# Kernel optimization log

Hardware: AMD Instinct MI355X
Metric: run time of the kernel (lower is better)

Reference implementation:

```python
import jax, jax.numpy as jnp
import numpy as np

# static config (matches init_kwargs)
H, W = 56, 56
T = 4            # temporal_dims
C = 256          # dim1
NH = 8           # num_heads
WS = 7           # window_size
SS = 3           # shift_size
HID = 1024       # mlp hidden = 4*C
N = WS * WS      # tokens per window
EPS = 1e-5


def _ln(x, g, b):
    m = jnp.mean(x, axis=-1, keepdims=True)
    v = jnp.mean((x - m) ** 2, axis=-1, keepdims=True)
    return (x - m) * jax.lax.rsqrt(v + EPS) * g + b


def _window_partition(x, ws):
    B, Hh, Ww, Cc = x.shape
    x = x.reshape(B, Hh // ws, ws, Ww // ws, ws, Cc)
    return x.transpose(0, 1, 3, 2, 4, 5).reshape(-1, ws, ws, Cc)


def _window_reverse(win, ws, Hh, Ww):
    B = win.shape[0] // ((Hh // ws) * (Ww // ws))
    x = win.reshape(B, Hh // ws, Ww // ws, ws, ws, -1)
    return x.transpose(0, 1, 3, 2, 4, 5).reshape(B, Hh, Ww, -1)


def _rel_pos_index(ws):
    coords = np.stack(np.meshgrid(np.arange(ws), np.arange(ws), indexing='ij'))
    cf = coords.reshape(2, -1)
    rel = (cf[:, :, None] - cf[:, None, :]).transpose(1, 2, 0).astype(np.int64)
    rel[..., 0] += ws - 1
    rel[..., 1] += ws - 1
    rel[..., 0] *= 2 * ws - 1
    return rel.sum(-1)  # (ws*ws, ws*ws)


def _shift_mask():
    # identical to the torch buffer built in __init__ (on temporal_dims*H x W grid)
    img = np.zeros((T * H, W), dtype=np.float32)
    cnt = 0
    for hs in (slice(0, -WS), slice(-WS, -SS), slice(-SS, None)):
        for wsl in (slice(0, -WS), slice(-WS, -SS), slice(-SS, None)):
            img[hs, wsl] = cnt
            cnt += 1
    mw = img.reshape((T * H) // WS, WS, W // WS, WS).transpose(0, 2, 1, 3).reshape(-1, N)
    am = mw[:, None, :] - mw[:, :, None]
    return np.where(am != 0, np.float32(-100.0), np.float32(0.0))  # (nW, N, N)

_RPI = _rel_pos_index(WS)
_ATTN_MASK = _shift_mask()


def setup_inputs() -> dict:
    key = jax.random.key(0)
    ks = jax.random.split(key, 8)
    B = 4
    s = 0.02
    return {
        'x1': jax.random.normal(ks[0], (B, T * H * W, C), jnp.float32),
        'x2': jax.random.normal(ks[1], (B, H * W, C), jnp.float32),
        'norm1_g': jnp.ones((C,), jnp.float32),
        'norm1_b': jnp.zeros((C,), jnp.float32),
        'qkv_w': jax.random.normal(ks[2], (3 * C, C), jnp.float32) * s,
        'qkv_b': jnp.zeros((3 * C,), jnp.float32),
        'proj_w': jax.random.normal(ks[3], (C, C), jnp.float32) * s,
        'proj_b': jnp.zeros((C,), jnp.float32),
        'rpb_table': jax.random.normal(ks[4], ((2 * WS - 1) ** 2, NH), jnp.float32) * s,
        'norm2_g': jnp.ones((C,), jnp.float32),
        'norm2_b': jnp.zeros((C,), jnp.float32),
        'fc1_w': jax.random.normal(ks[5], (HID, C), jnp.float32) * s,
        'fc1_b': jnp.zeros((HID,), jnp.float32),
        'fc2_w': jax.random.normal(ks[6], (C, HID), jnp.float32) * s,
        'fc2_b': jnp.zeros((C,), jnp.float32),
    }


def _block(x1, norm1_g, norm1_b, qkv_w, qkv_b, proj_w, proj_b, rpb_table,
           norm2_g, norm2_b, fc1_w, fc1_b, fc2_w, fc2_b):
    B, L, _ = x1.shape
    hd = C // NH
    shortcut = x1
    x = _ln(x1, norm1_g, norm1_b).reshape(B, T * H, W, C)
    # cyclic shift + window partition
    x = jnp.roll(x, shift=(-SS, -SS), axis=(1, 2))
    xw = _window_partition(x, WS).reshape(-1, N, C)          # (B*nW, N, C)
    Bw = xw.shape[0]
    nW = Bw // B
    # window attention with relative position bias + shift mask
    qkv = (xw @ qkv_w.T + qkv_b).reshape(Bw, N, 3, NH, hd).transpose(2, 0, 3, 1, 4)
    q, k, v = qkv[0], qkv[1], qkv[2]
    attn = jnp.einsum('bhnd,bhmd->bhnm', q * (hd ** -0.5), k)
    bias = rpb_table[jnp.asarray(_RPI)].transpose(2, 0, 1)    # (NH, N, N)
    attn = attn + bias[None]
    mask = jnp.asarray(_ATTN_MASK)
    attn = attn.reshape(B, nW, NH, N, N) + mask[None, :, None]
    attn = jax.nn.softmax(attn.reshape(Bw, NH, N, N), axis=-1)
    y = jnp.einsum('bhnm,bhmd->bhnd', attn, v).transpose(0, 2, 1, 3).reshape(Bw, N, C)
    y = y @ proj_w.T + proj_b
    # reverse windows + un-shift
    y = _window_reverse(y.reshape(-1, WS, WS, C), WS, T * H, W)
    y = jnp.roll(y, shift=(SS, SS), axis=(1, 2)).reshape(B, L, C)
    out = y
    x1 = shortcut + y
    # MLP (GELU exact, as torch nn.GELU default)
    h = _ln(x1, norm2_g, norm2_b)
    h = jax.nn.gelu(h @ fc1_w.T + fc1_b, approximate=False)
    x1 = x1 + (h @ fc2_w.T + fc2_b)
    return x1, out


def reference(x1, x2, norm1_g, norm1_b, qkv_w, qkv_b, proj_w, proj_b, rpb_table,
              norm2_g, norm2_b, fc1_w, fc1_b, fc2_w, fc2_b):
    # last_view=True: x2 is reshaped but unused by the executed path
    return _block(x1, norm1_g, norm1_b, qkv_w, qkv_b, proj_w, proj_b, rpb_table,
                  norm2_g, norm2_b, fc1_w, fc1_b, fc2_w, fc2_b)
```

## Files before the change

kernel.cpp:

```cpp
#include <hip/hip_runtime.h>
#include <hip/hip_bf16.h>
#include <cmath>

#define CDIM 256
#define TPW 49
#define NWIN 1024
#define MTOK (NWIN * TPW)
#define NHEAD 8
#define GH 224
#define GW 56
#define PLD 72

typedef __attribute__((ext_vector_type(8))) __bf16 bf16x8;
typedef __attribute__((ext_vector_type(4))) float f32x4;

__device__ __forceinline__ __bf16 to_bf16(float f) {
    __hip_bfloat16 h = __float2bfloat16(f);
    return *(__bf16*)&h;
}

__device__ __forceinline__ void async_copy16(const void* g, void* l) {
    __builtin_amdgcn_global_load_lds(
        (const __attribute__((address_space(1))) void*)g,
        (__attribute__((address_space(3))) void*)l, 16, 0, 0);
}

__device__ __forceinline__ float wave_sum(float v) {
    v += __shfl_down(v, 32);
    v += __shfl_down(v, 16);
    v += __shfl_down(v, 8);
    v += __shfl_down(v, 4);
    v += __shfl_down(v, 2);
    v += __shfl_down(v, 1);
    return v;
}

__global__ __launch_bounds__(256) void castall_kernel(
    const float* __restrict__ qw, const float* __restrict__ pw,
    const float* __restrict__ f1, const float* __restrict__ f2,
    __hip_bfloat16* __restrict__ dst)
{
    const int i = blockIdx.x * 256 + threadIdx.x;
    float v;
    if (i < 196608) v = qw[i];
    else if (i < 262144) v = pw[i - 196608];
    else if (i < 524288) v = f1[i - 262144];
    else v = f2[i - 524288];
    dst[i] = __float2bfloat16(v);
}

__global__ __launch_bounds__(256) void cb_kernel(
    const float* __restrict__ rpb, float* __restrict__ cbt)
{
    const int cls = blockIdx.x >> 3, head = blockIdx.x & 7;
    for (int e = threadIdx.x; e < 64 * 64; e += 256) {
        const int m = e >> 6, n = e & 63;
        float v;
        if (m >= 49 || n >= 49) v = -30000.0f;
        else {
            const int in_ = n / 7, jn = n - in_ * 7;
            const int im = m / 7, jm = m - im * 7;
            v = rpb[((in_ - im + 6) * 13 + (jn - jm + 6)) * 8 + head];
            const int hn = (cls & 2) ? 217 + in_ : in_;
            const int wn = (cls & 1) ? 49 + jn : jn;
            const int hm = (cls & 2) ? 217 + im : im;
            const int wm = (cls & 1) ? 49 + jm : jm;
            const int rn = (hn < 217 ? 0 : (hn < 221 ? 3 : 6)) + (wn < 49 ? 0 : (wn < 53 ? 1 : 2));
            const int rm = (hm < 217 ? 0 : (hm < 221 ? 3 : 6)) + (wm < 49 ? 0 : (wm < 53 ? 1 : 2));
            if (rn != rm) v -= 100.0f;
        }
        cbt[((long)blockIdx.x * 64 + m) * 64 + n] = v;
    }
}

__global__ __launch_bounds__(256) void ln1_window_kernel(
    const float* __restrict__ x1, const float* __restrict__ g,
    const float* __restrict__ b, __hip_bfloat16* __restrict__ out)
{
    const int wave = threadIdx.x >> 6, lane = threadIdx.x & 63;
    const int t = blockIdx.x * 4 + wave;
    const int bw = t / TPW, n = t - bw * TPW;
    const int bb = bw >> 8, wi = bw & 255;
    const int hb = wi >> 3, wb = wi & 7;
    const int i = n / 7, j = n - i * 7;
    int h0 = hb * 7 + i + 3; if (h0 >= GH) h0 -= GH;
    int w0 = wb * 7 + j + 3; if (w0 >= GW) w0 -= GW;
    const long src = ((long)(bb * GH + h0) * GW + w0) * CDIM + lane * 4;
    const float4 v = *(const float4*)(x1 + src);
    float s = v.x + v.y + v.z + v.w;
    s = wave_sum(s);
    const float mean = __shfl(s, 0) * (1.0f / 256.0f);
    const float4 d = { v.x - mean, v.y - mean, v.z - mean, v.w - mean };
    float s2 = d.x * d.x + d.y * d.y + d.z * d.z + d.w * d.w;
    s2 = wave_sum(s2);
    const float rstd = rsqrtf(__shfl(s2, 0) * (1.0f / 256.0f) + 1e-5f);
    const float4 g4 = *(const float4*)(g + lane * 4);
    const float4 b4 = *(const float4*)(b + lane * 4);
    short4 pk;
    { __bf16 h = to_bf16(d.x * rstd * g4.x + b4.x); pk.x = *(short*)&h; }
    { __bf16 h = to_bf16(d.y * rstd * g4.y + b4.y); pk.y = *(short*)&h; }
    { __bf16 h = to_bf16(d.z * rstd * g4.z + b4.z); pk.z = *(short*)&h; }
    { __bf16 h = to_bf16(d.w * rstd * g4.w + b4.w); pk.w = *(short*)&h; }
    *(short4*)((short*)out + (long)t * CDIM + lane * 4) = pk;
}

__global__ __launch_bounds__(256) void ln_kernel(
    const float* __restrict__ x, const float* __restrict__ g,
    const float* __restrict__ b, __hip_bfloat16* __restrict__ out)
{
    const int wave = threadIdx.x >> 6, lane = threadIdx.x & 63;
    const long t = (long)blockIdx.x * 4 + wave;
    const float4 v = *(const float4*)(x + t * CDIM + lane * 4);
    float s = v.x + v.y + v.z + v.w;
    s = wave_sum(s);
    const float mean = __shfl(s, 0) * (1.0f / 256.0f);
    const float4 d = { v.x - mean, v.y - mean, v.z - mean, v.w - mean };
    float s2 = d.x * d.x + d.y * d.y + d.z * d.z + d.w * d.w;
    s2 = wave_sum(s2);
    const float rstd = rsqrtf(__shfl(s2, 0) * (1.0f / 256.0f) + 1e-5f);
    const float4 g4 = *(const float4*)(g + lane * 4);
    const float4 b4 = *(const float4*)(b + lane * 4);
    short4 pk;
    { __bf16 h = to_bf16(d.x * rstd * g4.x + b4.x); pk.x = *(short*)&h; }
    { __bf16 h = to_bf16(d.y * rstd * g4.y + b4.y); pk.y = *(short*)&h; }
    { __bf16 h = to_bf16(d.z * rstd * g4.z + b4.z); pk.z = *(short*)&h; }
    { __bf16 h = to_bf16(d.w * rstd * g4.w + b4.w); pk.w = *(short*)&h; }
    *(short4*)((short*)out + t * CDIM + lane * 4) = pk;
}

template <int EPI, typename OutT>
__global__ __launch_bounds__(256) void gemm_mfma(
    const __hip_bfloat16* __restrict__ X, const __hip_bfloat16* __restrict__ W,
    const float* __restrict__ bias, OutT* __restrict__ Y,
    int M, int K, int N, const float* __restrict__ res, float* __restrict__ Y2)
{
    __shared__ __hip_bfloat16 As[128 * 32];
    __shared__ __hip_bfloat16 Bs[128 * 32];
    const int tid = threadIdx.x;
    const int wave = tid >> 6, lane = tid & 63;
    const int nwg = gridDim.x * gridDim.y;
    const int L = blockIdx.y * gridDim.x + blockIdx.x;
    const int cpx = nwg >> 3;
    const int orig = (L & 7) * cpx + (L >> 3);
    const int bxx = orig % gridDim.x;
    const int byy = orig / gridDim.x;
    const int bm = byy * 128, bn = bxx * 128;
    const int wm = (wave & 1) * 64, wn = (wave >> 1) * 64;
    const int m16 = lane & 15, quad = lane >> 4;
    const int srow = lane >> 2;
    const int scol = (lane & 3) * 8;

    f32x4 acc[4][4] = {};

    for (int k0 = 0; k0 < K; k0 += 32) {
#pragma unroll
        for (int j = 0; j < 2; ++j) {
            const int rg = wave * 2 + j;
            const int row = rg * 16 + srow;
            async_copy16(X + (long)(bm + row) * K + k0 + scol, (char*)As + rg * 1024);
            async_copy16(W + (long)(bn + row) * K + k0 + scol, (char*)Bs + rg * 1024);
        }
        __syncthreads();
        bf16x8 af[4], bf[4];
#pragma unroll
        for (int i = 0; i < 4; ++i)
            af[i] = *(const bf16x8*)&As[(wm + i * 16 + m16) * 32 + quad * 8];
#pragma unroll
        for (int j = 0; j < 4; ++j)
            bf[j] = *(const bf16x8*)&Bs[(wn + j * 16 + m16) * 32 + quad * 8];
#pragma unroll
        for (int i = 0; i < 4; ++i)
#pragma unroll
            for (int j = 0; j < 4; ++j)
                acc[i][j] = __builtin_amdgcn_mfma_f32_16x16x32_bf16(bf[j], af[i], acc[i][j], 0, 0, 0);
        __syncthreads();
    }

#pragma unroll
    for (int i = 0; i < 4; ++i) {
        const long row = bm + wm + i * 16 + m16;
        long drow = row;
        if (EPI == 3) {
            const unsigned t = (unsigned)row;
            const unsigned bw_ = t / 49u;
            const unsigned n_ = t - bw_ * 49u;
            const unsigned bb = bw_ >> 8, wi = bw_ & 255u;
            const unsigned hb = wi >> 3, wbl = wi & 7u;
            const unsigned ii = n_ / 7u, jj = n_ - ii * 7u;
            int h0 = hb * 7 + ii + 3; if (h0 >= GH) h0 -= GH;
            int w0 = wbl * 7 + jj + 3; if (w0 >= GW) w0 -= GW;
            drow = (long)bb * (GH * GW) + h0 * GW + w0;
        }
#pragma unroll
        for (int j = 0; j < 4; ++j) {
            const int col = bn + wn + j * 16 + quad * 4;
            const float4 b4 = *(const float4*)&bias[col];
            float v[4];
            v[0] = acc[i][j][0] + b4.x;
            v[1] = acc[i][j][1] + b4.y;
            v[2] = acc[i][j][2] + b4.z;
            v[3] = acc[i][j][3] + b4.w;
            if (EPI == 1) {
#pragma unroll
                for (int r = 0; r < 4; ++r)
                    v[r] = 0.5f * v[r] * (1.0f + erff(v[r] * 0.70710678118654752f));
            }
            if (EPI == 0 || EPI == 1) {
                short4 pk;
                { __bf16 h = to_bf16(v[0]); pk.x = *(short*)&h; }
                { __bf16 h = to_bf16(v[1]); pk.y = *(short*)&h; }
                { __bf16 h = to_bf16(v[2]); pk.z = *(short*)&h; }
                { __bf16 h = to_bf16(v[3]); pk.w = *(short*)&h; }
                *(short4*)((short*)Y + row * N + col) = pk;
            } else if (EPI == 2) {
                const float4 r4 = *(const float4*)(res + row * N + col);
                float4 o4 = { v[0] + r4.x, v[1] + r4.y, v[2] + r4.z, v[3] + r4.w };
                *(float4*)((float*)Y + row * N + col) = o4;
            } else if (EPI == 3) {
                const long a = drow * 256 + col;
                const float4 x4 = *(const float4*)(res + a);
                float4 y4 = { v[0], v[1], v[2], v[3] };
                *(float4*)(Y2 + a) = y4;
                float4 s4 = { v[0] + x4.x, v[1] + x4.y, v[2] + x4.z, v[3] + x4.w };
                *(float4*)((float*)Y + a) = s4;
            }
        }
    }
}

__global__ __launch_bounds__(256) void attn_mfma_kernel(
    const __hip_bfloat16* __restrict__ qkv,
    const float* __restrict__ cbt,
    __hip_bfloat16* __restrict__ yout)
{
    __shared__ __bf16 P[4][64][PLD];
    const int tid = threadIdx.x;
    const int wave = tid >> 6, lane = tid & 63;
    const int bw = blockIdx.x >> 1;
    const int head = (blockIdx.x & 1) * 4 + wave;
    const int m16 = lane & 15, quad = lane >> 4;
    const int wi = bw & 255;
    const int hb = wi >> 3, wb = wi & 7;
    const int cls = ((hb == 31) ? 2 : 0) + ((wb == 7) ? 1 : 0);

    const __bf16* qb = (const __bf16*)qkv + (long)bw * TPW * 768 + head * 32;

    bf16x8 qf[4], kf[4];
#pragma unroll
    for (int i = 0; i < 4; ++i) {
        const int n = i * 16 + m16;
        bf16x8 q = {}, k = {};
        if (n < TPW) {
            const __bf16* p = qb + (long)n * 768 + quad * 8;
            q = *(const bf16x8*)p;
            k = *(const bf16x8*)(p + 256);
        }
        qf[i] = q; kf[i] = k;
    }

    bf16x8 vf[2][2];
#pragma unroll
    for (int jt = 0; jt < 2; ++jt)
#pragma unroll
        for (int kt = 0; kt < 2; ++kt) {
            bf16x8 v = {};
#pragma unroll
            for (int j = 0; j < 8; ++j) {
                const int tok = kt * 32 + quad * 8 + j;
                if (tok < TPW) v[j] = qb[(long)tok * 768 + 512 + jt * 16 + m16];
            }
            vf[jt][kt] = v;
        }

    f32x4 s[4][4] = {};
#pragma unroll
    for (int i = 0; i < 4; ++i)
#pragma unroll
        for (int j = 0; j < 4; ++j)
            s[i][j] = __builtin_amdgcn_mfma_f32_16x16x32_bf16(qf[i], kf[j], s[i][j], 0, 0, 0);

    const float* cb = cbt + (long)(cls * 8 + head) * 64 * 64;
#pragma unroll
    for (int j = 0; j < 4; ++j) {
        const int m = j * 16 + m16;
#pragma unroll
        for (int i = 0; i < 4; ++i) {
            const float4 c = *(const float4*)(cb + m * 64 + i * 16 + quad * 4);
            s[i][j][0] = s[i][j][0] * 0.17677669529663687f + c.x;
            s[i][j][1] = s[i][j][1] * 0.17677669529663687f + c.y;
            s[i][j][2] = s[i][j][2] * 0.17677669529663687f + c.z;
            s[i][j][3] = s[i][j][3] * 0.17677669529663687f + c.w;
        }
    }

#pragma unroll
    for (int i = 0; i < 4; ++i) {
#pragma unroll
        for (int r = 0; r < 4; ++r) {
            float mx = fmaxf(fmaxf(s[i][0][r], s[i][1][r]), fmaxf(s[i][2][r], s[i][3][r]));
            mx = fmaxf(mx, __shfl_xor(mx, 1));
            mx = fmaxf(mx, __shfl_xor(mx, 2));
            mx = fmaxf(mx, __shfl_xor(mx, 4));
            mx = fmaxf(mx, __shfl_xor(mx, 8));
            float sum = 0.0f;
#pragma unroll
            for (int j = 0; j < 4; ++j) {
                const float e = __expf(s[i][j][r] - mx);
                s[i][j][r] = e;
                sum += e;
            }
            sum += __shfl_xor(sum, 1);
            sum += __shfl_xor(sum, 2);
            sum += __shfl_xor(sum, 4);
            sum += __shfl_xor(sum, 8);
            const float inv = 1.0f / sum;
#pragma unroll
            for (int j = 0; j < 4; ++j)
                P[wave][i * 16 + quad * 4 + r][j * 16 + m16] = to_bf16(s[i][j][r] * inv);
        }
    }

    f32x4 o[4][2] = {};
#pragma unroll
    for (int kt = 0; kt < 2; ++kt)
#pragma unroll
        for (int i = 0; i < 4; ++i) {
            const bf16x8 pf = *(const bf16x8*)&P[wave][i * 16 + m16][kt * 32 + quad * 8];
#pragma unroll
            for (int jt = 0; jt < 2; ++jt)
                o[i][jt] = __builtin_amdgcn_mfma_f32_16x16x32_bf16(vf[jt][kt], pf, o[i][jt], 0, 0, 0);
        }

#pragma unroll
    for (int i = 0; i < 4; ++i) {
        const int tok = i * 16 + m16;
        if (tok < TPW) {
#pragma unroll
            for (int jt = 0; jt < 2; ++jt) {
                short4 pk;
                { __bf16 h = to_bf16(o[i][jt][0]); pk.x = *(short*)&h; }
                { __bf16 h = to_bf16(o[i][jt][1]); pk.y = *(short*)&h; }
                { __bf16 h = to_bf16(o[i][jt][2]); pk.z = *(short*)&h; }
                { __bf16 h = to_bf16(o[i][jt][3]); pk.w = *(short*)&h; }
                *(short4*)((short*)yout + ((long)bw * TPW + tok) * CDIM + head * 32 + jt * 16 + quad * 4) = pk;
            }
        }
    }
}

extern "C" void kernel_launch(void* const* d_in, const int* in_sizes, int n_in,
                              void* d_out, int out_size, void* d_ws, size_t ws_size,
                              hipStream_t stream) {
    (void)in_sizes; (void)n_in; (void)out_size; (void)ws_size;
    const float* x1     = (const float*)d_in[0];
    const float* n1g    = (const float*)d_in[2];
    const float* n1b    = (const float*)d_in[3];
    const float* qkv_w  = (const float*)d_in[4];
    const float* qkv_b  = (const float*)d_in[5];
    const float* proj_w = (const float*)d_in[6];
    const float* proj_b = (const float*)d_in[7];
    const float* rpb    = (const float*)d_in[8];
    const float* n2g    = (const float*)d_in[9];
    const float* n2b    = (const float*)d_in[10];
    const float* fc1_w  = (const float*)d_in[11];
    const float* fc1_b  = (const float*)d_in[12];
    const float* fc2_w  = (const float*)d_in[13];
    const float* fc2_b  = (const float*)d_in[14];

    float* out_x1 = (float*)d_out;
    float* out_y  = out_x1 + (long)MTOK * CDIM;

    char* ws = (char*)d_ws;
    const size_t SZ_A   = (size_t)MTOK * CDIM * sizeof(__hip_bfloat16);
    const size_t SZ_BIG = (size_t)MTOK * 1024 * sizeof(__hip_bfloat16);
    __hip_bfloat16* A    = (__hip_bfloat16*)ws;
    char*           BIG  = ws + SZ_A;
    __hip_bfloat16* qkvb = (__hip_bfloat16*)BIG;
    __hip_bfloat16* H1   = (__hip_bfloat16*)BIG;
    __hip_bfloat16* wB   = (__hip_bfloat16*)(ws + SZ_A + SZ_BIG);
    __hip_bfloat16* qkv_wb  = wB;
    __hip_bfloat16* proj_wb = wB + 196608;
    __hip_bfloat16* fc1_wb  = wB + 262144;
    __hip_bfloat16* fc2_wb  = wB + 524288;
    float* cbt = (float*)(wB + 786432);

    castall_kernel<<<3072, 256, 0, stream>>>(qkv_w, proj_w, fc1_w, fc2_w, wB);
    cb_kernel<<<32, 256, 0, stream>>>(rpb, cbt);
    ln1_window_kernel<<<MTOK / 4, 256, 0, stream>>>(x1, n1g, n1b, A);
    gemm_mfma<0, __hip_bfloat16><<<dim3(768 / 128, MTOK / 128), 256, 0, stream>>>(
        A, qkv_wb, qkv_b, qkvb, MTOK, CDIM, 768, nullptr, nullptr);
    attn_mfma_kernel<<<NWIN * 2, 256, 0, stream>>>(qkvb, cbt, A);
    gemm_mfma<3, float><<<dim3(256 / 128, MTOK / 128), 256, 0, stream>>>(
        A, proj_wb, proj_b, out_x1, MTOK, CDIM, CDIM, x1, out_y);
    ln_kernel<<<MTOK / 4, 256, 0, stream>>>(out_x1, n2g, n2b, A);
    gemm_mfma<1, __hip_bfloat16><<<dim3(1024 / 128, MTOK / 128), 256, 0, stream>>>(
        A, fc1_wb, fc1_b, H1, MTOK, CDIM, 1024, nullptr, nullptr);
    gemm_mfma<2, float><<<dim3(256 / 128, MTOK / 128), 256, 0, stream>>>(
        H1, fc2_wb, fc2_b, out_x1, MTOK, 1024, CDIM, out_x1, nullptr);
}
```

Baseline: 457.8 us.

## Fuse MLP fc1+GELU+fc2 into one kernel keeping hidden activations in LDS

Replaces the separate fc1 GEMM (writing a bf16 hidden tensor to global memory) and fc2 GEMM with a single kernel. Each 64-row block loops over 16 hidden chunks of 64, computes fc1 plus GELU into LDS, and accumulates fc2 into registers before adding bias and the residual. This removes the global write and read of the large hidden activation tensor. In exchange each block reloads all fc1/fc2 weights, the loop is serialised by syncthreads with no double buffering, and the tile is smaller (64 rows), so MFMA utilisation and weight traffic may suffer.

Result: slower. 477.2 us (+4.2%).

```diff
diff --git a/kernel.cpp b/kernel.cpp
--- a/kernel.cpp
+++ b/kernel.cpp
@@ -228,6 +228,116 @@
     }
 }
 
+__global__ __launch_bounds__(256) void fused_mlp_kernel(
+    const __hip_bfloat16* __restrict__ A,
+    const __hip_bfloat16* __restrict__ W1,
+    const float* __restrict__ b1,
+    const __hip_bfloat16* __restrict__ W2,
+    const float* __restrict__ b2,
+    float* __restrict__ io)
+{
+    __shared__ __hip_bfloat16 Wbuf[16384];
+    __shared__ char Hb[8192];
+    const int tid = threadIdx.x;
+    const int wave = tid >> 6, lane = tid & 63;
+    const int m16 = lane & 15, quad = lane >> 4;
+    const int L = blockIdx.x;
+    const int orig = (L & 7) * 98 + (L >> 3);
+    const long bm = (long)orig * 64;
+
+    const int lr = wave * 16 + m16;
+    const int swz = (lr & 7) << 4;
+
+    bf16x8 af[8];
+    const __hip_bfloat16* arow = A + (bm + lr) * 256 + quad * 8;
+#pragma unroll
+    for (int kk = 0; kk < 8; ++kk)
+        af[kk] = *(const bf16x8*)(arow + kk * 32);
+
+    f32x4 acc2[16] = {};
+
+    for (int c = 0; c < 16; ++c) {
+        {
+            const __hip_bfloat16* src = W1 + (long)c * 64 * 256;
+#pragma unroll
+            for (int r = 0; r < 8; ++r) {
+                const int s = (tid << 4) + (r << 12);
+                const int row = s >> 9;
+                const int g = ((s >> 4) & 31) ^ (row & 7);
+                async_copy16(src + row * 256 + g * 8,
+                             (char*)Wbuf + (r << 12) + wave * 1024);
+            }
+        }
+        __syncthreads();
+        f32x4 s1[4] = {};
+#pragma unroll
+        for (int kk = 0; kk < 8; ++kk) {
+#pragma unroll
+            for (int j = 0; j < 4; ++j) {
+                const int n = j * 16 + m16;
+                const int off = n * 512 + ((kk * 64 + quad * 16) ^ ((n & 7) << 4));
+                const bf16x8 wf = *(const bf16x8*)((const char*)Wbuf + off);
+                s1[j] = __builtin_amdgcn_mfma_f32_16x16x32_bf16(wf, af[kk], s1[j], 0, 0, 0);
+            }
+        }
+        __syncthreads();
+        {
+            const __hip_bfloat16* src = W2 + c * 64;
+#pragma unroll
+            for (int r = 0; r < 8; ++r) {
+                const int s = (tid << 4) + (r << 12);
+                const int row = s >> 7;
+                const int g = ((s >> 4) & 7) ^ (row & 7);
+                async_copy16(src + (long)row * 1024 + g * 8,
+                             (char*)Wbuf + (r << 12) + wave * 1024);
+            }
+        }
+#pragma unroll
+        for (int j = 0; j < 4; ++j) {
+            const float4 bb = *(const float4*)(b1 + c * 64 + j * 16 + quad * 4);
+            float v[4];
+            v[0] = s1[j][0] + bb.x; v[1] = s1[j][1] + bb.y;
+            v[2] = s1[j][2] + bb.z; v[3] = s1[j][3] + bb.w;
+#pragma unroll
+            for (int r = 0; r < 4; ++r)
+                v[r] = 0.5f * v[r] * (1.0f + erff(v[r] * 0.70710678118654752f));
+            short4 pk;
+            { __bf16 h = to_bf16(v[0]); pk.x = *(short*)&h; }
+            { __bf16 h = to_bf16(v[1]); pk.y = *(short*)&h; }
+            { __bf16 h = to_bf16(v[2]); pk.z = *(short*)&h; }
+            { __bf16 h = to_bf16(v[3]); pk.w = *(short*)&h; }
+            const int off = lr * 128 + ((j * 32 + quad * 8) ^ swz);
+            *(short4*)(Hb + off) = pk;
+        }
+        __syncthreads();
+#pragma unroll
+        for (int kk = 0; kk < 2; ++kk) {
+            const int hoff = lr * 128 + ((kk * 64 + quad * 16) ^ swz);
+            const bf16x8 hf = *(const bf16x8*)(Hb + hoff);
+#pragma unroll
+            for (int f = 0; f < 16; ++f) {
+                const int nn = f * 16 + m16;
+                const int off = nn * 128 + ((kk * 64 + quad * 16) ^ ((nn & 7) << 4));
+                const bf16x8 wf = *(const bf16x8*)((const char*)Wbuf + off);
+                acc2[f] = __builtin_amdgcn_mfma_f32_16x16x32_bf16(wf, hf, acc2[f], 0, 0, 0);
+            }
+        }
+        __syncthreads();
+    }
+
+    const long grow = bm + lr;
+#pragma unroll
+    for (int f = 0; f < 16; ++f) {
+        const int col = f * 16 + quad * 4;
+        const float4 bb = *(const float4*)(b2 + col);
+        const long a = grow * 256 + col;
+        const float4 r4 = *(const float4*)(io + a);
+        float4 o4 = { acc2[f][0] + bb.x + r4.x, acc2[f][1] + bb.y + r4.y,
+                      acc2[f][2] + bb.z + r4.z, acc2[f][3] + bb.w + r4.w };
+        *(float4*)(io + a) = o4;
+    }
+}
+
 __global__ __launch_bounds__(256) void attn_mfma_kernel(
     const __hip_bfloat16* __restrict__ qkv,
     const float* __restrict__ cbt,
@@ -376,7 +486,6 @@
     __hip_bfloat16* A    = (__hip_bfloat16*)ws;
     char*           BIG  = ws + SZ_A;
     __hip_bfloat16* qkvb = (__hip_bfloat16*)BIG;
-    __hip_bfloat16* H1   = (__hip_bfloat16*)BIG;
     __hip_bfloat16* wB   = (__hip_bfloat16*)(ws + SZ_A + SZ_BIG);
     __hip_bfloat16* qkv_wb  = wB;
     __hip_bfloat16* proj_wb = wB + 196608;
@@ -393,8 +502,6 @@
     gemm_mfma<3, float><<<dim3(256 / 128, MTOK / 128), 256, 0, stream>>>(
         A, proj_wb, proj_b, out_x1, MTOK, CDIM, CDIM, x1, out_y);
     ln_kernel<<<MTOK / 4, 256, 0, stream>>>(out_x1, n2g, n2b, A);
-    gemm_mfma<1, __hip_bfloat16><<<dim3(1024 / 128, MTOK / 128), 256, 0, stream>>>(
-        A, fc1_wb, fc1_b, H1, MTOK, CDIM, 1024, nullptr, nullptr);
-    gemm_mfma<2, float><<<dim3(256 / 128, MTOK / 128), 256, 0, stream>>>(
-        H1, fc2_wb, fc2_b, out_x1, MTOK, 1024, CDIM, out_x1, nullptr);
-}
+    fused_mlp_kernel<<<MTOK / 64, 256, 0, stream>>>(
+        A, fc1_wb, fc1_b, fc2_wb, fc2_b, out_x1);
+}
```

## Double-buffer LDS tiles in MFMA GEMM to overlap loads with compute

Applied to the files above, without the earlier changes.

Adds a second LDS buffer for the A and B tiles and issues the async global-to-LDS copies for the next K step before the MFMA work on the current one. This lets the global load latency hide behind the matrix math and removes one barrier per iteration. In exchange LDS use per block doubles, which may reduce occupancy, and correctness depends on the async loads having completed once the single barrier at the end of each iteration passes.

Result: no change. 463.0 us (+1.1%).

```diff
diff --git a/kernel.cpp b/kernel.cpp
--- a/kernel.cpp
+++ b/kernel.cpp
@@ -134,8 +134,8 @@
     const float* __restrict__ bias, OutT* __restrict__ Y,
     int M, int K, int N, const float* __restrict__ res, float* __restrict__ Y2)
 {
-    __shared__ __hip_bfloat16 As[128 * 32];
-    __shared__ __hip_bfloat16 Bs[128 * 32];
+    __shared__ __hip_bfloat16 As[2][128 * 32];
+    __shared__ __hip_bfloat16 Bs[2][128 * 32];
     const int tid = threadIdx.x;
     const int wave = tid >> 6, lane = tid & 63;
     const int nwg = gridDim.x * gridDim.y;
@@ -150,30 +150,42 @@
     const int srow = lane >> 2;
     const int scol = (lane & 3) * 8;
 
+    const __hip_bfloat16* xb = X + (long)bm * K + scol;
+    const __hip_bfloat16* wb = W + (long)bn * K + scol;
+    const int rg0 = wave * 2, rg1 = wave * 2 + 1;
+    const long xr0 = (long)(rg0 * 16 + srow) * K, xr1 = (long)(rg1 * 16 + srow) * K;
+
     f32x4 acc[4][4] = {};
 
+    async_copy16(xb + xr0, (char*)As[0] + rg0 * 1024);
+    async_copy16(wb + xr0, (char*)Bs[0] + rg0 * 1024);
+    async_copy16(xb + xr1, (char*)As[0] + rg1 * 1024);
+    async_copy16(wb + xr1, (char*)Bs[0] + rg1 * 1024);
+    __syncthreads();
+
+    int cur = 0;
     for (int k0 = 0; k0 < K; k0 += 32) {
-#pragma unroll
-        for (int j = 0; j < 2; ++j) {
-            const int rg = wave * 2 + j;
-            const int row = rg * 16 + srow;
-            async_copy16(X + (long)(bm + row) * K + k0 + scol, (char*)As + rg * 1024);
-            async_copy16(W + (long)(bn + row) * K + k0 + scol, (char*)Bs + rg * 1024);
-        }
-        __syncthreads();
+        if (k0 + 32 < K) {
+            const int nxt = cur ^ 1;
+            async_copy16(xb + xr0 + k0 + 32, (char*)As[nxt] + rg0 * 1024);
+            async_copy16(wb + xr0 + k0 + 32, (char*)Bs[nxt] + rg0 * 1024);
+            async_copy16(xb + xr1 + k0 + 32, (char*)As[nxt] + rg1 * 1024);
+            async_copy16(wb + xr1 + k0 + 32, (char*)Bs[nxt] + rg1 * 1024);
+        }
         bf16x8 af[4], bf[4];
 #pragma unroll
         for (int i = 0; i < 4; ++i)
-            af[i] = *(const bf16x8*)&As[(wm + i * 16 + m16) * 32 + quad * 8];
+            af[i] = *(const bf16x8*)&As[cur][(wm + i * 16 + m16) * 32 + quad * 8];
 #pragma unroll
         for (int j = 0; j < 4; ++j)
-            bf[j] = *(const bf16x8*)&Bs[(wn + j * 16 + m16) * 32 + quad * 8];
+            bf[j] = *(const bf16x8*)&Bs[cur][(wn + j * 16 + m16) * 32 + quad * 8];
 #pragma unroll
         for (int i = 0; i < 4; ++i)
 #pragma unroll
             for (int j = 0; j < 4; ++j)
                 acc[i][j] = __builtin_amdgcn_mfma_f32_16x16x32_bf16(bf[j], af[i], acc[i][j], 0, 0, 0);
         __syncthreads();
+        cur ^= 1;
     }
 
 #pragma unroll
```
